# Kernel optimization log

Hardware: AMD Instinct MI355X
Metric: run time of the kernel (lower is better)

## Reference

```python
import jax, jax.numpy as jnp
import numpy as np

N_NODES = 50000
N_EDGES = 800000
IN_X = 64
IN_E = 32
HID = 64
NUM_GRAPHS = 50
EPS = 1e-5


def setup_inputs() -> dict:
    key = jax.random.key(0)
    ks = jax.random.split(key, 16)
    x = jax.random.normal(ks[0], (N_NODES, IN_X), dtype=jnp.float32)
    edge_index = jax.random.randint(ks[1], (2, N_EDGES), 0, N_NODES, dtype=jnp.int32)
    edge_attr = jax.random.normal(ks[2], (N_EDGES, IN_E), dtype=jnp.float32)
    batch = jnp.sort(jax.random.randint(ks[3], (N_NODES,), 0, NUM_GRAPHS, dtype=jnp.int32))
    s1 = 1.0 / np.sqrt(IN_X + IN_E)
    s2 = 1.0 / np.sqrt(HID + IN_E)
    sr = 1.0 / np.sqrt(IN_X)
    sh = 1.0 / np.sqrt(HID)
    return {
        "x": x, "edge_index": edge_index, "edge_attr": edge_attr, "batch": batch,
        "Wn1": jax.random.uniform(ks[4], (IN_X + IN_E, HID), jnp.float32, -s1, s1),
        "bn1": jax.random.uniform(ks[5], (HID,), jnp.float32, -s1, s1),
        "Wr1": jax.random.uniform(ks[6], (IN_X, HID), jnp.float32, -sr, sr),
        "g1": jnp.ones((HID,), jnp.float32), "be1": jnp.zeros((HID,), jnp.float32),
        "Wn2": jax.random.uniform(ks[7], (HID + IN_E, HID), jnp.float32, -s2, s2),
        "bn2": jax.random.uniform(ks[8], (HID,), jnp.float32, -s2, s2),
        "Wr2": jax.random.uniform(ks[9], (HID, HID), jnp.float32, -sh, sh),
        "g2": jnp.ones((HID,), jnp.float32), "be2": jnp.zeros((HID,), jnp.float32),
        "Wro": jax.random.uniform(ks[10], (HID, 1), jnp.float32, -sh, sh),
        "bro": jax.random.uniform(ks[11], (1,), jnp.float32, -sh, sh),
    }


def _edge_sage_conv(x, src, dst, edge_attr, Wn, bn, Wr):
    # message: concat(x_j, edge_attr) -> linear -> relu  (per-edge, [E, hid])
    m = jax.nn.relu(jnp.concatenate([x[src], edge_attr], axis=-1) @ Wn + bn)
    # scatter-mean onto destination nodes
    s = jax.ops.segment_sum(m, dst, num_segments=N_NODES)
    cnt = jax.ops.segment_sum(jnp.ones((dst.shape[0],), m.dtype), dst, num_segments=N_NODES)
    aggr = s / jnp.maximum(cnt, 1.0)[:, None]
    return x @ Wr + aggr


def _batchnorm(x, gamma, beta):
    mu = jnp.mean(x, axis=0)
    var = jnp.mean(jnp.square(x - mu), axis=0)  # biased var, training-mode BN
    return gamma * (x - mu) * jax.lax.rsqrt(var + EPS) + beta


def reference(x, edge_index, edge_attr, batch, Wn1, bn1, Wr1, g1, be1,
              Wn2, bn2, Wr2, g2, be2, Wro, bro):
    src, dst = edge_index[0], edge_index[1]
    h = _edge_sage_conv(x, src, dst, edge_attr, Wn1, bn1, Wr1)
    h = jax.nn.relu(_batchnorm(h, g1, be1))
    h = _edge_sage_conv(h, src, dst, edge_attr, Wn2, bn2, Wr2)
    h = jax.nn.relu(_batchnorm(h, g2, be2))
    # global mean pool per graph
    s = jax.ops.segment_sum(h, batch, num_segments=NUM_GRAPHS)
    cnt = jax.ops.segment_sum(jnp.ones((h.shape[0],), h.dtype), batch, num_segments=NUM_GRAPHS)
    hg = s / jnp.maximum(cnt, 1.0)[:, None]
    return (hg @ Wro + bro).squeeze(-1)
```

## Files before the change

### kernel.cpp

```cpp
#include <hip/hip_runtime.h>

#define N_NODES   50000
#define N_EDGES   800000
#define HID       64
#define NUM_GRAPHS 50
#define EPS       1e-5f
#define NWT       3125
#define NBC       782
#define NHPAD     50176
#define SCAN_B    98
#define NBKT      98
#define BSH       9
#define BATCH     2048

typedef __attribute__((ext_vector_type(8))) short short8;
typedef __attribute__((ext_vector_type(4))) float f32x4;

__device__ __forceinline__ unsigned short bfbits(float x) {
    __bf16 h = (__bf16)x;
    return __builtin_bit_cast(unsigned short, h);
}
__device__ __forceinline__ short8 cvt8hi(const float4& a, const float4& b) {
    float f[8] = {a.x, a.y, a.z, a.w, b.x, b.y, b.z, b.w};
    short8 hi;
#pragma unroll
    for (int i = 0; i < 8; ++i) hi[i] = (short)bfbits(f[i]);
    return hi;
}

__global__ __launch_bounds__(256) void k_hist(const int* __restrict__ dst,
                                              int* __restrict__ ihist) {
    int tid = blockIdx.x * blockDim.x + threadIdx.x;
    int stride = gridDim.x * blockDim.x;
    for (int e = tid; e < N_EDGES; e += stride) atomicAdd(&ihist[dst[e]], 1);
}

__global__ __launch_bounds__(512) void k_scan1(const int* __restrict__ ihist,
                                               int* __restrict__ off,
                                               int* __restrict__ bsum) {
    __shared__ int s[512];
    const int t = threadIdx.x, i = blockIdx.x * 512 + t;
    const int v = ihist[i];
    s[t] = v;
    __syncthreads();
    for (int o = 1; o < 512; o <<= 1) {
        int u = (t >= o) ? s[t - o] : 0;
        __syncthreads();
        s[t] += u;
        __syncthreads();
    }
    off[i] = s[t] - v;
    if (t == 511) bsum[blockIdx.x] = s[t];
}

__global__ void k_scan2(const int* __restrict__ bsum, int* __restrict__ bscan) {
    if (threadIdx.x == 0) {
        int acc = 0;
        for (int b = 0; b < SCAN_B; ++b) { bscan[b] = acc; acc += bsum[b]; }
    }
}

__global__ __launch_bounds__(512) void k_scan3(int* __restrict__ off,
                                               const int* __restrict__ bscan) {
    const int i = blockIdx.x * 512 + threadIdx.x;
    off[i] += bscan[i >> 9];
}

__global__ void k_bcur(const int* __restrict__ off, int* __restrict__ bcur) {
    int b = threadIdx.x;
    if (b < NBKT) bcur[b] = off[b << BSH];
}

__global__ __launch_bounds__(256) void k_bin(const int* __restrict__ src,
                                             const int* __restrict__ dst,
                                             int* __restrict__ bcur,
                                             int2* __restrict__ binned) {
    __shared__ int bh[NBKT], gb[NBKT];
    const int tid = threadIdx.x;
    const int base = blockIdx.x * BATCH + tid * 8;
    int2 rec[8]; int bk[8]; bool val[8];
#pragma unroll
    for (int j = 0; j < 8; ++j) {
        const int e = base + j;
        val[j] = e < N_EDGES;
        if (val[j]) {
            const int d = dst[e];
            rec[j] = int2{src[e] | (d << 16), e};
            bk[j] = d >> BSH;
        } else bk[j] = 0;
    }
    if (tid < NBKT) bh[tid] = 0;
    __syncthreads();
#pragma unroll
    for (int j = 0; j < 8; ++j) if (val[j]) atomicAdd(&bh[bk[j]], 1);
    __syncthreads();
    if (tid < NBKT) { gb[tid] = atomicAdd(&bcur[tid], bh[tid]); bh[tid] = 0; }
    __syncthreads();
#pragma unroll
    for (int j = 0; j < 8; ++j)
        if (val[j]) {
            const int r = atomicAdd(&bh[bk[j]], 1);
            binned[gb[bk[j]] + r] = rec[j];
        }
}

__global__ __launch_bounds__(256) void k_sortb(const int2* __restrict__ binned,
                                               const int* __restrict__ off,
                                               int2* __restrict__ epk) {
    __shared__ int cur[512];
    const int b = blockIdx.x;
    const int nbase = b << BSH;
    const int tid = threadIdx.x;
    for (int i = tid; i < 512; i += 256) cur[i] = off[nbase + i];
    const int start = off[nbase];
    const int end = (b == NBKT - 1) ? N_EDGES : off[nbase + 512];
    __syncthreads();
    for (int p = start + tid; p < end; p += 256) {
        const int2 r = binned[p];
        const int d = ((unsigned)r.x) >> 16;
        const int pos = atomicAdd(&cur[d - nbase], 1);
        epk[pos] = r;
    }
}

__global__ __launch_bounds__(256) void k_prepEA(const float* __restrict__ ea,
                                                unsigned short* __restrict__ eaB) {
    int t = blockIdx.x * blockDim.x + threadIdx.x;
    if (t >= N_EDGES * 4) return;
    float4 a = *(const float4*)(ea + (size_t)t * 8);
    float4 b = *(const float4*)(ea + (size_t)t * 8 + 4);
    *(short8*)(eaB + (size_t)t * 8) = cvt8hi(a, b);
}

__global__ void k_gcnt(const int* __restrict__ batch, float* __restrict__ gcnt) {
    int g = threadIdx.x;
    if (g >= NUM_GRAPHS) return;
    auto lb = [&](int val) {
        int lo = 0, hi = N_NODES;
        while (lo < hi) { int mid = (lo + hi) >> 1; if (batch[mid] < val) lo = mid + 1; else hi = mid; }
        return lo;
    };
    gcnt[g] = (float)(lb(g + 1) - lb(g));
}

__global__ void k_prepW(const float* __restrict__ W, unsigned short* __restrict__ Wb) {
    int t = blockIdx.x * blockDim.x + threadIdx.x;
    if (t >= 96 * 64) return;
    int k = t >> 6, n = t & 63;
    Wb[n * 104 + k] = bfbits(W[t]);
}

__global__ void k_prepWr(const float* __restrict__ Wr, unsigned short* __restrict__ Wrb) {
    int t = blockIdx.x * blockDim.x + threadIdx.x;
    if (t >= 64 * 64) return;
    int k = t >> 6, n = t & 63;
    Wrb[n * 64 + k] = bfbits(Wr[t]);
}

__global__ __launch_bounds__(256) void k_prepX(const float* __restrict__ x,
                                               unsigned short* __restrict__ xb) {
    int t = blockIdx.x * blockDim.x + threadIdx.x;
    if (t >= N_NODES * 8) return;
    float4 a = ((const float4*)(x + (size_t)t * 8))[0];
    float4 b = ((const float4*)(x + (size_t)t * 8))[1];
    *(short8*)(xb + (size_t)t * 8) = cvt8hi(a, b);
}

__global__ __launch_bounds__(256) void k_prepH(const float* __restrict__ h,
                                               const float* __restrict__ ss,
                                               unsigned short* __restrict__ hb) {
    int t = blockIdx.x * blockDim.x + threadIdx.x;
    if (t >= N_NODES * 8) return;
    const int f0 = (t & 7) * 8;
    float4 sca = *(const float4*)(ss + f0);
    float4 scb = *(const float4*)(ss + f0 + 4);
    float4 sha = *(const float4*)(ss + 64 + f0);
    float4 shb = *(const float4*)(ss + 64 + f0 + 4);
    const float* r = h + (size_t)t * 8;
    float4 a = ((const float4*)r)[0];
    float4 b = ((const float4*)r)[1];
    a.x = fmaxf(a.x * sca.x + sha.x, 0.f);
    a.y = fmaxf(a.y * sca.y + sha.y, 0.f);
    a.z = fmaxf(a.z * sca.z + sha.z, 0.f);
    a.w = fmaxf(a.w * sca.w + sha.w, 0.f);
    b.x = fmaxf(b.x * scb.x + shb.x, 0.f);
    b.y = fmaxf(b.y * scb.y + shb.y, 0.f);
    b.z = fmaxf(b.z * scb.z + shb.z, 0.f);
    b.w = fmaxf(b.w * scb.w + shb.w, 0.f);
    *(short8*)(hb + (size_t)t * 8) = cvt8hi(a, b);
}

__global__ __launch_bounds__(256) void k_edge(const unsigned short* __restrict__ xb,
                                              const unsigned short* __restrict__ eaB,
                                              const int2* __restrict__ epk,
                                              const unsigned short* __restrict__ Wb,
                                              const float* __restrict__ bias,
                                              float* __restrict__ aggr) {
    __shared__ int ldstw[4][2][16];

    const int tid  = threadIdx.x;
    const int lane = tid & 63;
    const int w    = tid >> 6;
    const int ew   = (blockIdx.x * 4 + w) * 32;

    const int fr   = lane & 15;
    const int hi4  = lane >> 4;
    const int koff = hi4 * 8;
    const int rb   = hi4 * 4;

    if (lane < 32)
        ldstw[w][lane >> 4][lane & 15] = ((unsigned)epk[ew + lane].x) >> 16;

    const int2 eA = epk[ew + fr];
    const int2 eB = epk[ew + 16 + fr];
    const int sA = eA.x & 0xffff, iA = eA.y;
    const int sB = eB.x & 0xffff, iB = eB.y;

    short8 aA0 = *(const short8*)(xb + (size_t)sA * 64 + koff);
    short8 aA1 = *(const short8*)(xb + (size_t)sA * 64 + 32 + koff);
    short8 aA2 = *(const short8*)(eaB + (size_t)iA * 32 + koff);
    short8 aB0 = *(const short8*)(xb + (size_t)sB * 64 + koff);
    short8 aB1 = *(const short8*)(xb + (size_t)sB * 64 + 32 + koff);
    short8 aB2 = *(const short8*)(eaB + (size_t)iB * 32 + koff);

    f32x4 accA[4], accB[4];
#pragma unroll
    for (int n = 0; n < 4; ++n) {
        const float bv = bias[n * 16 + fr];
        accA[n] = f32x4{bv, bv, bv, bv};
        accB[n] = f32x4{bv, bv, bv, bv};
    }

#pragma unroll
    for (int kb = 0; kb < 3; ++kb) {
        const short8 aA = (kb == 0) ? aA0 : (kb == 1) ? aA1 : aA2;
        const short8 aB = (kb == 0) ? aB0 : (kb == 1) ? aB1 : aB2;
#pragma unroll
        for (int nn = 0; nn < 4; ++nn) {
            const short8 bh = *(const short8*)(Wb + (nn * 16 + fr) * 104 + kb * 32 + koff);
            accA[nn] = __builtin_amdgcn_mfma_f32_16x16x32_bf16(aA, bh, accA[nn], 0, 0, 0);
            accB[nn] = __builtin_amdgcn_mfma_f32_16x16x32_bf16(aB, bh, accB[nn], 0, 0, 0);
        }
    }

#pragma unroll
    for (int n = 0; n < 4; ++n)
#pragma unroll
        for (int j = 0; j < 4; ++j) {
            accA[n][j] = fmaxf(accA[n][j], 0.f);
            accB[n][j] = fmaxf(accB[n][j], 0.f);
        }

#define SEGREDUCE(TT, ACC)                                                    \
    {                                                                         \
        int r = 0;                                                            \
        while (r < 16) {                                                      \
            const int d = ldstw[w][TT][r];                                    \
            int e2 = r + 1;                                                   \
            while (e2 < 16 && ldstw[w][TT][e2] == d) ++e2;                    \
            float v0 = 0.f, v1 = 0.f, v2 = 0.f, v3 = 0.f;                     \
            _Pragma("unroll")                                                 \
            for (int j = 0; j < 4; ++j) {                                     \
                const bool in = (rb + j >= r) && (rb + j < e2);               \
                v0 += in ? ACC[0][j] : 0.f;                                   \
                v1 += in ? ACC[1][j] : 0.f;                                   \
                v2 += in ? ACC[2][j] : 0.f;                                   \
                v3 += in ? ACC[3][j] : 0.f;                                   \
            }                                                                 \
            v0 += __shfl_xor(v0, 16); v0 += __shfl_xor(v0, 32);               \
            v1 += __shfl_xor(v1, 16); v1 += __shfl_xor(v1, 32);               \
            v2 += __shfl_xor(v2, 16); v2 += __shfl_xor(v2, 32);               \
            v3 += __shfl_xor(v3, 16); v3 += __shfl_xor(v3, 32);               \
            const float val = hi4 == 0 ? v0 : hi4 == 1 ? v1 : hi4 == 2 ? v2 : v3; \
            unsafeAtomicAdd(&aggr[(size_t)d * 64 + lane], val);               \
            r = e2;                                                           \
        }                                                                     \
    }
    SEGREDUCE(0, accA)
    SEGREDUCE(1, accB)
#undef SEGREDUCE
}

__global__ __launch_bounds__(256) void k_combine(const unsigned short* __restrict__ xbin,
                                                 const unsigned short* __restrict__ Wrb,
                                                 const float* __restrict__ aggr,
                                                 const int*   __restrict__ ihist,
                                                 float* __restrict__ h,
                                                 float* __restrict__ partial) {
    __shared__ float ssum[4][64];
    __shared__ float ssq[4][64];

    const int tid  = threadIdx.x;
    const int lane = tid & 63;
    const int w    = tid >> 6;
    const int wt   = blockIdx.x * 4 + w;
    const int fr   = lane & 15;
    const int hi4  = lane >> 4;
    const int koff = hi4 * 8;
    const int rb   = hi4 * 4;

    float rs[4] = {0.f, 0.f, 0.f, 0.f};
    float rq[4] = {0.f, 0.f, 0.f, 0.f};

    if (wt < NWT) {
        const int n0 = wt * 16;
        const short8 a0 = *(const short8*)(xbin + (size_t)(n0 + fr) * 64 + koff);
        const short8 a1 = *(const short8*)(xbin + (size_t)(n0 + fr) * 64 + 32 + koff);
        f32x4 acc[4] = {};
#pragma unroll
        for (int kb = 0; kb < 2; ++kb) {
            const short8 a = kb == 0 ? a0 : a1;
#pragma unroll
            for (int nn = 0; nn < 4; ++nn) {
                const short8 bh = *(const short8*)(Wrb + (nn * 16 + fr) * 64 + kb * 32 + koff);
                acc[nn] = __builtin_amdgcn_mfma_f32_16x16x32_bf16(a, bh, acc[nn], 0, 0, 0);
            }
        }
        const int4 degs = *(const int4*)(ihist + n0 + rb);
#pragma unroll
        for (int j = 0; j < 4; ++j) {
            const int dg = (&degs.x)[j];
            const float invc = 1.0f / fmaxf((float)dg, 1.0f);
            const int row = n0 + rb + j;
#pragma unroll
            for (int nn = 0; nn < 4; ++nn) {
                const float v = acc[nn][j] + aggr[(size_t)row * 64 + nn * 16 + fr] * invc;
                h[(size_t)row * 64 + nn * 16 + fr] = v;
                rs[nn] += v;
                rq[nn] += v * v;
            }
        }
    }

#pragma unroll
    for (int nn = 0; nn < 4; ++nn) {
        rs[nn] += __shfl_xor(rs[nn], 16); rs[nn] += __shfl_xor(rs[nn], 32);
        rq[nn] += __shfl_xor(rq[nn], 16); rq[nn] += __shfl_xor(rq[nn], 32);
    }
    if (hi4 == 0) {
#pragma unroll
        for (int nn = 0; nn < 4; ++nn) {
            ssum[w][nn * 16 + fr] = rs[nn];
            ssq[w][nn * 16 + fr]  = rq[nn];
        }
    }
    __syncthreads();
    if (tid < 64) {
        partial[blockIdx.x * 128 + tid] =
            ssum[0][tid] + ssum[1][tid] + ssum[2][tid] + ssum[3][tid];
    } else if (tid < 128) {
        int l = tid - 64;
        partial[blockIdx.x * 128 + 64 + l] =
            ssq[0][l] + ssq[1][l] + ssq[2][l] + ssq[3][l];
    }
}

__global__ void k_bnfin(const float* __restrict__ partial, const float* __restrict__ g,
                        const float* __restrict__ be, float* __restrict__ ss) {
    __shared__ float tot[128];
    int t = threadIdx.x;
    float s = 0.f;
    for (int b = 0; b < NBC; ++b) s += partial[b * 128 + t];
    tot[t] = s;
    __syncthreads();
    if (t < 64) {
        float mu  = tot[t] * (1.0f / (float)N_NODES);
        float var = tot[64 + t] * (1.0f / (float)N_NODES) - mu * mu;
        float sc  = g[t] * rsqrtf(var + EPS);
        ss[t]      = sc;
        ss[64 + t] = be[t] - mu * sc;
    }
}

__global__ __launch_bounds__(256) void k_bnpool(const float* __restrict__ h,
                                                const float* __restrict__ ss,
                                                const int* __restrict__ batch,
                                                float* __restrict__ gsum) {
    const int lane = threadIdx.x & 63;
    const int wid  = (blockIdx.x * blockDim.x + threadIdx.x) >> 6;
    const int nw   = (gridDim.x * blockDim.x) >> 6;
    const float sc = ss[lane];
    const float sh = ss[64 + lane];
    const int chunk = (N_NODES + nw - 1) / nw;
    const int n0 = wid * chunk;
    const int n1 = min(n0 + chunk, N_NODES);
    int curg = -1;
    float acc = 0.f;
    for (int n = n0; n < n1; ++n) {
        int g = __builtin_amdgcn_readfirstlane(batch[n]);
        if (g != curg) {
            if (curg >= 0) unsafeAtomicAdd(&gsum[curg * 64 + lane], acc);
            curg = g;
            acc = 0.f;
        }
        acc += fmaxf(h[(size_t)n * 64 + lane] * sc + sh, 0.f);
    }
    if (curg >= 0) unsafeAtomicAdd(&gsum[curg * 64 + lane], acc);
}

__global__ void k_final(const float* __restrict__ gsum, const float* __restrict__ gcnt,
                        const float* __restrict__ Wro, const float* __restrict__ bro,
                        float* __restrict__ out) {
    int g = blockIdx.x;
    int lane = threadIdx.x;
    float v = gsum[g * 64 + lane] / fmaxf(gcnt[g], 1.0f) * Wro[lane];
#pragma unroll
    for (int off = 32; off > 0; off >>= 1) v += __shfl_down(v, off, 64);
    if (lane == 0) out[g] = v + bro[0];
}

extern "C" void kernel_launch(void* const* d_in, const int* in_sizes, int n_in,
                              void* d_out, int out_size, void* d_ws, size_t ws_size,
                              hipStream_t stream) {
    (void)in_sizes; (void)n_in; (void)out_size; (void)ws_size;
    const float* x    = (const float*)d_in[0];
    const int*   ei   = (const int*)d_in[1];
    const float* ea   = (const float*)d_in[2];
    const int*   batch= (const int*)d_in[3];
    const float* Wn1  = (const float*)d_in[4];
    const float* bn1  = (const float*)d_in[5];
    const float* Wr1  = (const float*)d_in[6];
    const float* g1   = (const float*)d_in[7];
    const float* be1  = (const float*)d_in[8];
    const float* Wn2  = (const float*)d_in[9];
    const float* bn2  = (const float*)d_in[10];
    const float* Wr2  = (const float*)d_in[11];
    const float* g2   = (const float*)d_in[12];
    const float* be2  = (const float*)d_in[13];
    const float* Wro  = (const float*)d_in[14];
    const float* bro  = (const float*)d_in[15];
    const int* src = ei;
    const int* dst = ei + N_EDGES;

    float* ws = (float*)d_ws;
    float* gsum   = ws;
    float* aggr   = gsum + 3200;
    int*   ihist  = (int*)(aggr + (size_t)N_NODES * 64);
    const size_t zero_floats = 3200 + (size_t)N_NODES * 64 + NHPAD;
    float* h      = (float*)(ihist + NHPAD);
    float* gcnt   = h + (size_t)N_NODES * 64;
    float* part1  = gcnt + 64;
    float* part2  = part1 + NBC * 128;
    float* ss1    = part2 + NBC * 128;
    float* ss2    = ss1 + 128;
    unsigned short* Wb1  = (unsigned short*)(ss2 + 128);
    unsigned short* Wb2  = Wb1 + 6656;
    unsigned short* Wrb1 = Wb2 + 6656;
    unsigned short* Wrb2 = Wrb1 + 4096;
    int* off     = (int*)(Wrb2 + 4096);
    int* bsum    = off + NHPAD;
    int* bscan   = bsum + 128;
    int* bcur    = bscan + 128;
    int2* epk    = (int2*)(bcur + 128);
    int2* binned = epk + N_EDGES;
    unsigned short* xb  = (unsigned short*)(binned + N_EDGES);
    unsigned short* hb  = xb + (size_t)N_NODES * 64;
    unsigned short* eaB = hb + (size_t)N_NODES * 64;

    hipMemsetAsync(d_ws, 0, zero_floats * sizeof(float), stream);

    k_hist<<<512, 256, 0, stream>>>(dst, ihist);
    k_scan1<<<SCAN_B, 512, 0, stream>>>(ihist, off, bsum);
    k_scan2<<<1, 64, 0, stream>>>(bsum, bscan);
    k_scan3<<<SCAN_B, 512, 0, stream>>>(off, bscan);
    k_bcur<<<1, 128, 0, stream>>>(off, bcur);
    k_bin<<<(N_EDGES + BATCH - 1) / BATCH, 256, 0, stream>>>(src, dst, bcur, binned);
    k_sortb<<<NBKT, 256, 0, stream>>>(binned, off, epk);
    k_prepEA<<<N_EDGES * 4 / 256, 256, 0, stream>>>(ea, eaB);

    k_gcnt<<<1, 64, 0, stream>>>(batch, gcnt);
    k_prepW<<<24, 256, 0, stream>>>(Wn1, Wb1);
    k_prepW<<<24, 256, 0, stream>>>(Wn2, Wb2);
    k_prepWr<<<16, 256, 0, stream>>>(Wr1, Wrb1);
    k_prepWr<<<16, 256, 0, stream>>>(Wr2, Wrb2);
    k_prepX<<<(N_NODES * 8 + 255) / 256, 256, 0, stream>>>(x, xb);

    k_edge<<<N_EDGES / 128, 256, 0, stream>>>(xb, eaB, epk, Wb1, bn1, aggr);
    k_combine<<<NBC, 256, 0, stream>>>(xb, Wrb1, aggr, ihist, h, part1);
    k_bnfin<<<1, 128, 0, stream>>>(part1, g1, be1, ss1);
    k_prepH<<<(N_NODES * 8 + 255) / 256, 256, 0, stream>>>(h, ss1, hb);

    hipMemsetAsync(aggr, 0, (size_t)N_NODES * 64 * sizeof(float), stream);
    k_edge<<<N_EDGES / 128, 256, 0, stream>>>(hb, eaB, epk, Wb2, bn2, aggr);
    k_combine<<<NBC, 256, 0, stream>>>(hb, Wrb2, aggr, ihist, h, part2);
    k_bnfin<<<1, 128, 0, stream>>>(part2, g2, be2, ss2);

    k_bnpool<<<256, 256, 0, stream>>>(h, ss2, batch, gsum);
    k_final<<<NUM_GRAPHS, 64, 0, stream>>>(gsum, gcnt, Wro, bro, (float*)d_out);
}
```

Measured before the change: 315.4 us.

## Pre-permute edge attributes into sorted order and merge small prep kernels

Edge attributes are now gathered into dst-sorted order once, in a prep pass that converts them to bf16, so both edge passes read them contiguously instead of by scattered edge id. The packed edge record is split into separate src/dst and edge-id arrays. The bcur kernel is folded into scan3, the weight, count and x conversions are merged into one launch, and the second aggr memset is replaced by zeroing aggr inside combine. This cuts launch count and memory traffic, at the cost of a gather pass over edge attributes.

```diff
diff --git a/kernel.cpp b/kernel.cpp
--- a/kernel.cpp
+++ b/kernel.cpp
@@ -7,6 +7,7 @@
 #define EPS       1e-5f
 #define NWT       3125
 #define NBC       782
+#define NPX       1563
 #define NHPAD     50176
 #define SCAN_B    98
 #define NBKT      98
@@ -61,14 +62,12 @@
 }
 
 __global__ __launch_bounds__(512) void k_scan3(int* __restrict__ off,
-                                               const int* __restrict__ bscan) {
+                                               const int* __restrict__ bscan,
+                                               int* __restrict__ bcur) {
     const int i = blockIdx.x * 512 + threadIdx.x;
-    off[i] += bscan[i >> 9];
-}
-
-__global__ void k_bcur(const int* __restrict__ off, int* __restrict__ bcur) {
-    int b = threadIdx.x;
-    if (b < NBKT) bcur[b] = off[b << BSH];
+    const int v = off[i] + bscan[i >> 9];
+    off[i] = v;
+    if ((i & 511) == 0) bcur[i >> 9] = v;
 }
 
 __global__ __launch_bounds__(256) void k_bin(const int* __restrict__ src,
@@ -106,7 +105,8 @@
 
 __global__ __launch_bounds__(256) void k_sortb(const int2* __restrict__ binned,
                                                const int* __restrict__ off,
-                                               int2* __restrict__ epk) {
+                                               int* __restrict__ epk,
+                                               int* __restrict__ seid) {
     __shared__ int cur[512];
     const int b = blockIdx.x;
     const int nbase = b << BSH;
@@ -119,51 +119,62 @@
         const int2 r = binned[p];
         const int d = ((unsigned)r.x) >> 16;
         const int pos = atomicAdd(&cur[d - nbase], 1);
-        epk[pos] = r;
-    }
-}
-
-__global__ __launch_bounds__(256) void k_prepEA(const float* __restrict__ ea,
-                                                unsigned short* __restrict__ eaB) {
+        epk[pos] = r.x;
+        seid[pos] = r.y;
+    }
+}
+
+__global__ __launch_bounds__(256) void k_prepEAS(const float* __restrict__ ea,
+                                                 const int* __restrict__ seid,
+                                                 unsigned short* __restrict__ eaS) {
     int t = blockIdx.x * blockDim.x + threadIdx.x;
     if (t >= N_EDGES * 4) return;
-    float4 a = *(const float4*)(ea + (size_t)t * 8);
-    float4 b = *(const float4*)(ea + (size_t)t * 8 + 4);
-    *(short8*)(eaB + (size_t)t * 8) = cvt8hi(a, b);
-}
-
-__global__ void k_gcnt(const int* __restrict__ batch, float* __restrict__ gcnt) {
-    int g = threadIdx.x;
-    if (g >= NUM_GRAPHS) return;
-    auto lb = [&](int val) {
-        int lo = 0, hi = N_NODES;
-        while (lo < hi) { int mid = (lo + hi) >> 1; if (batch[mid] < val) lo = mid + 1; else hi = mid; }
-        return lo;
-    };
-    gcnt[g] = (float)(lb(g + 1) - lb(g));
-}
-
-__global__ void k_prepW(const float* __restrict__ W, unsigned short* __restrict__ Wb) {
-    int t = blockIdx.x * blockDim.x + threadIdx.x;
-    if (t >= 96 * 64) return;
-    int k = t >> 6, n = t & 63;
-    Wb[n * 104 + k] = bfbits(W[t]);
-}
-
-__global__ void k_prepWr(const float* __restrict__ Wr, unsigned short* __restrict__ Wrb) {
-    int t = blockIdx.x * blockDim.x + threadIdx.x;
-    if (t >= 64 * 64) return;
-    int k = t >> 6, n = t & 63;
-    Wrb[n * 64 + k] = bfbits(Wr[t]);
-}
-
-__global__ __launch_bounds__(256) void k_prepX(const float* __restrict__ x,
-                                               unsigned short* __restrict__ xb) {
-    int t = blockIdx.x * blockDim.x + threadIdx.x;
-    if (t >= N_NODES * 8) return;
-    float4 a = ((const float4*)(x + (size_t)t * 8))[0];
-    float4 b = ((const float4*)(x + (size_t)t * 8))[1];
-    *(short8*)(xb + (size_t)t * 8) = cvt8hi(a, b);
+    const int p = t >> 2, q = t & 3;
+    const int eid = seid[p];
+    float4 a = *(const float4*)(ea + (size_t)eid * 32 + q * 8);
+    float4 b = *(const float4*)(ea + (size_t)eid * 32 + q * 8 + 4);
+    *(short8*)(eaS + (size_t)p * 32 + q * 8) = cvt8hi(a, b);
+}
+
+__global__ __launch_bounds__(256) void k_prep(const float* __restrict__ x,
+                                              unsigned short* __restrict__ xb,
+                                              const int* __restrict__ batch,
+                                              float* __restrict__ gcnt,
+                                              const float* __restrict__ Wn1,
+                                              const float* __restrict__ Wn2,
+                                              unsigned short* __restrict__ Wb1,
+                                              unsigned short* __restrict__ Wb2,
+                                              const float* __restrict__ Wr1,
+                                              const float* __restrict__ Wr2,
+                                              unsigned short* __restrict__ Wrb1,
+                                              unsigned short* __restrict__ Wrb2) {
+    const int tid = threadIdx.x;
+    if (blockIdx.x < NPX) {
+        int t = blockIdx.x * 256 + tid;
+        if (t >= N_NODES * 8) return;
+        float4 a = ((const float4*)(x + (size_t)t * 8))[0];
+        float4 b = ((const float4*)(x + (size_t)t * 8))[1];
+        *(short8*)(xb + (size_t)t * 8) = cvt8hi(a, b);
+        return;
+    }
+    if (tid < NUM_GRAPHS) {
+        auto lb = [&](int val) {
+            int lo = 0, hi = N_NODES;
+            while (lo < hi) { int mid = (lo + hi) >> 1; if (batch[mid] < val) lo = mid + 1; else hi = mid; }
+            return lo;
+        };
+        gcnt[tid] = (float)(lb(tid + 1) - lb(tid));
+    }
+    for (int t = tid; t < 96 * 64; t += 256) {
+        int k = t >> 6, n = t & 63;
+        Wb1[n * 104 + k] = bfbits(Wn1[t]);
+        Wb2[n * 104 + k] = bfbits(Wn2[t]);
+    }
+    for (int t = tid; t < 64 * 64; t += 256) {
+        int k = t >> 6, n = t & 63;
+        Wrb1[n * 64 + k] = bfbits(Wr1[t]);
+        Wrb2[n * 64 + k] = bfbits(Wr2[t]);
+    }
 }
 
 __global__ __launch_bounds__(256) void k_prepH(const float* __restrict__ h,
@@ -191,8 +202,8 @@
 }
 
 __global__ __launch_bounds__(256) void k_edge(const unsigned short* __restrict__ xb,
-                                              const unsigned short* __restrict__ eaB,
-                                              const int2* __restrict__ epk,
+                                              const unsigned short* __restrict__ eaS,
+                                              const int* __restrict__ epk,
                                               const unsigned short* __restrict__ Wb,
                                               const float* __restrict__ bias,
                                               float* __restrict__ aggr) {
@@ -209,19 +220,19 @@
     const int rb   = hi4 * 4;
 
     if (lane < 32)
-        ldstw[w][lane >> 4][lane & 15] = ((unsigned)epk[ew + lane].x) >> 16;
-
-    const int2 eA = epk[ew + fr];
-    const int2 eB = epk[ew + 16 + fr];
-    const int sA = eA.x & 0xffff, iA = eA.y;
-    const int sB = eB.x & 0xffff, iB = eB.y;
+        ldstw[w][lane >> 4][lane & 15] = ((unsigned)epk[ew + lane]) >> 16;
+
+    const int sdA = epk[ew + fr];
+    const int sdB = epk[ew + 16 + fr];
+    const int sA = sdA & 0xffff;
+    const int sB = sdB & 0xffff;
 
     short8 aA0 = *(const short8*)(xb + (size_t)sA * 64 + koff);
     short8 aA1 = *(const short8*)(xb + (size_t)sA * 64 + 32 + koff);
-    short8 aA2 = *(const short8*)(eaB + (size_t)iA * 32 + koff);
+    short8 aA2 = *(const short8*)(eaS + (size_t)(ew + fr) * 32 + koff);
     short8 aB0 = *(const short8*)(xb + (size_t)sB * 64 + koff);
     short8 aB1 = *(const short8*)(xb + (size_t)sB * 64 + 32 + koff);
-    short8 aB2 = *(const short8*)(eaB + (size_t)iB * 32 + koff);
+    short8 aB2 = *(const short8*)(eaS + (size_t)(ew + 16 + fr) * 32 + koff);
 
     f32x4 accA[4], accB[4];
 #pragma unroll
@@ -283,7 +294,7 @@
 
 __global__ __launch_bounds__(256) void k_combine(const unsigned short* __restrict__ xbin,
                                                  const unsigned short* __restrict__ Wrb,
-                                                 const float* __restrict__ aggr,
+                                                 float* __restrict__ aggr,
                                                  const int*   __restrict__ ihist,
                                                  float* __restrict__ h,
                                                  float* __restrict__ partial) {
@@ -324,8 +335,11 @@
             const int row = n0 + rb + j;
 #pragma unroll
             for (int nn = 0; nn < 4; ++nn) {
-                const float v = acc[nn][j] + aggr[(size_t)row * 64 + nn * 16 + fr] * invc;
-                h[(size_t)row * 64 + nn * 16 + fr] = v;
+                const size_t ai = (size_t)row * 64 + nn * 16 + fr;
+                const float av = aggr[ai];
+                aggr[ai] = 0.f;
+                const float v = acc[nn][j] + av * invc;
+                h[ai] = v;
                 rs[nn] += v;
                 rq[nn] += v * v;
             }
@@ -451,37 +465,32 @@
     int* bsum    = off + NHPAD;
     int* bscan   = bsum + 128;
     int* bcur    = bscan + 128;
-    int2* epk    = (int2*)(bcur + 128);
-    int2* binned = epk + N_EDGES;
-    unsigned short* xb  = (unsigned short*)(binned + N_EDGES);
+    int2* binned = (int2*)(bcur + 128);
+    int* epk     = (int*)(binned + N_EDGES);
+    int* seid    = epk + N_EDGES;
+    unsigned short* xb  = (unsigned short*)(seid + N_EDGES);
     unsigned short* hb  = xb + (size_t)N_NODES * 64;
-    unsigned short* eaB = hb + (size_t)N_NODES * 64;
+    unsigned short* eaS = hb + (size_t)N_NODES * 64;
 
     hipMemsetAsync(d_ws, 0, zero_floats * sizeof(float), stream);
 
     k_hist<<<512, 256, 0, stream>>>(dst, ihist);
     k_scan1<<<SCAN_B, 512, 0, stream>>>(ihist, off, bsum);
     k_scan2<<<1, 64, 0, stream>>>(bsum, bscan);
-    k_scan3<<<SCAN_B, 512, 0, stream>>>(off, bscan);
-    k_bcur<<<1, 128, 0, stream>>>(off, bcur);
+    k_scan3<<<SCAN_B, 512, 0, stream>>>(off, bscan, bcur);
     k_bin<<<(N_EDGES + BATCH - 1) / BATCH, 256, 0, stream>>>(src, dst, bcur, binned);
-    k_sortb<<<NBKT, 256, 0, stream>>>(binned, off, epk);
-    k_prepEA<<<N_EDGES * 4 / 256, 256, 0, stream>>>(ea, eaB);
-
-    k_gcnt<<<1, 64, 0, stream>>>(batch, gcnt);
-    k_prepW<<<24, 256, 0, stream>>>(Wn1, Wb1);
-    k_prepW<<<24, 256, 0, stream>>>(Wn2, Wb2);
-    k_prepWr<<<16, 256, 0, stream>>>(Wr1, Wrb1);
-    k_prepWr<<<16, 256, 0, stream>>>(Wr2, Wrb2);
-    k_prepX<<<(N_NODES * 8 + 255) / 256, 256, 0, stream>>>(x, xb);
-
-    k_edge<<<N_EDGES / 128, 256, 0, stream>>>(xb, eaB, epk, Wb1, bn1, aggr);
+    k_sortb<<<NBKT, 256, 0, stream>>>(binned, off, epk, seid);
+    k_prepEAS<<<N_EDGES * 4 / 256, 256, 0, stream>>>(ea, seid, eaS);
+
+    k_prep<<<NPX + 1, 256, 0, stream>>>(x, xb, batch, gcnt,
+                                        Wn1, Wn2, Wb1, Wb2, Wr1, Wr2, Wrb1, Wrb2);
+
+    k_edge<<<N_EDGES / 128, 256, 0, stream>>>(xb, eaS, epk, Wb1, bn1, aggr);
     k_combine<<<NBC, 256, 0, stream>>>(xb, Wrb1, aggr, ihist, h, part1);
     k_bnfin<<<1, 128, 0, stream>>>(part1, g1, be1, ss1);
     k_prepH<<<(N_NODES * 8 + 255) / 256, 256, 0, stream>>>(h, ss1, hb);
 
-    hipMemsetAsync(aggr, 0, (size_t)N_NODES * 64 * sizeof(float), stream);
-    k_edge<<<N_EDGES / 128, 256, 0, stream>>>(hb, eaB, epk, Wb2, bn2, aggr);
+    k_edge<<<N_EDGES / 128, 256, 0, stream>>>(hb, eaS, epk, Wb2, bn2, aggr);
     k_combine<<<NBC, 256, 0, stream>>>(hb, Wrb2, aggr, ihist, h, part2);
     k_bnfin<<<1, 128, 0, stream>>>(part2, g2, be2, ss2);
 
```

Measured after the change: 317.0 us (median of 2 runs). About the same (+0.5%).
